# Performance work log

Measured on AMD Instinct MI355X. Metric: run time of the kernel, lower is better.

## Reference

```python
import jax, jax.numpy as jnp
import numpy as np

N, N_UP, I, L, K = 32, 16, 128, 4, 16
H_S, H_D = 4 * I, 4          # single / double stream widths (512, 4)
F_LEN = 3 * H_S + 2 * H_D    # 1544


def setup_inputs() -> dict:
    key = jax.random.key(0)
    ks = jax.random.split(key, 11)
    f32 = jnp.float32
    return {
        "electron_positions": jax.random.normal(ks[0], (N, 3), f32),
        "nuclei_positions": jax.random.normal(ks[1], (I, 3), f32),
        # torch.rand-style U[0,1) params, scaled to avoid tanh saturation / det overflow
        "v_matrices": jax.random.uniform(ks[2], (L, N, F_LEN, H_S), f32) * 1e-3,
        "b_vectors": jax.random.uniform(ks[3], (L, N, H_S), f32),
        "w_matrices": jax.random.uniform(ks[4], (L, N, N, H_D, H_D), f32) * 0.1,
        "c_vectors": jax.random.uniform(ks[5], (L, N, N, H_D), f32),
        "final_weights": jax.random.uniform(ks[6], (K, N, H_S), f32) * 1e-3,
        "final_biases": jax.random.uniform(ks[7], (K, N), f32),
        "pi_weights": jax.random.uniform(ks[8], (K, N, I), f32) * 1e-2,
        "sigma_weights": jax.random.uniform(ks[9], (K, N, I), f32),
        "omega_weights": jax.random.uniform(ks[10], (K,), f32),
    }


def _fermi_layer(V, b, W, c, sh, dh):
    # sh: [N, H_S], dh: [N, N, H_D]
    g_up = jnp.mean(sh[:N_UP], axis=0)          # [H_S]
    g_dn = jnp.mean(sh[N_UP:], axis=0)          # [H_S]
    dg_up = jnp.mean(dh[:, :N_UP], axis=1)      # [N, H_D]
    dg_dn = jnp.mean(dh[:, N_UP:], axis=1)      # [N, H_D]
    f = jnp.concatenate(
        [sh,
         jnp.broadcast_to(g_up, (N, H_S)),
         jnp.broadcast_to(g_dn, (N, H_S)),
         dg_up, dg_dn], axis=1)                 # [N, F_LEN]
    so = jnp.tanh(jnp.einsum('nfo,nf->no', V, f) + b)      # per-electron matvec
    if so.shape == sh.shape:
        so = so + sh                            # residual (shapes always match here)
    # torch bmm(W[b,i,j], h[b,j]) -> out[b,i] = sum_j W[b,i,j] h[b,j]
    do = jnp.tanh(jnp.einsum('mnij,mnj->mni', W, dh) + c)
    if do.shape == dh.shape:
        do = do + dh
    return so, do


def _forward(electron_positions, nuclei_positions, v_matrices, b_vectors,
             w_matrices, c_vectors, final_weights, final_biases,
             pi_weights, sigma_weights, omega_weights):
    eN = electron_positions[:, None, :] - nuclei_positions[None, :, :]   # [N, I, 3]
    eN_norm = jnp.linalg.norm(eN, axis=-1)                               # [N, I]
    sh = jnp.concatenate([eN.reshape(N, 3 * I), eN_norm], axis=1)        # [N, 4I]
    ee = electron_positions[:, None, :] - electron_positions[None, :, :] # [N, N, 3]
    ee_norm = jnp.linalg.norm(ee, axis=-1, keepdims=True)                # [N, N, 1]
    dh = jnp.concatenate([ee, ee_norm], axis=-1)                         # [N, N, 4]

    # Source quirk: applies layers 0..L-2, then layer L-2 again; layers[-1] unused.
    for li in list(range(L - 1)) + [L - 2]:
        sh, dh = _fermi_layer(v_matrices[li], b_vectors[li],
                              w_matrices[li], c_vectors[li], sh, dh)

    # phi[k,i,j] = (w_ki . h_j + b_ki) * sum_m pi_kim * exp(-||sigma_kim * eN_jm||)
    fd = jnp.einsum('kid,jd->kij', final_weights, sh) + final_biases[:, :, None]
    # ||sigma * v|| = |sigma| * ||v||
    env_exp = jnp.exp(-jnp.abs(sigma_weights)[:, :, None, :]
                      * eN_norm[None, None, :, :])                        # [K,N,N,I]
    env = jnp.einsum('kim,kijm->kij', pi_weights, env_exp)                # [K,N,N]
    phi = fd * env
    d_up = jnp.linalg.det(phi[:, :N_UP, :N_UP])
    d_dn = jnp.linalg.det(phi[:, N_UP:, N_UP:])
    return jnp.sum(omega_weights * d_up * d_dn)


def reference(electron_positions, nuclei_positions, v_matrices, b_vectors,
              w_matrices, c_vectors, final_weights, final_biases,
              pi_weights, sigma_weights, omega_weights):
    return _forward(electron_positions, nuclei_positions, v_matrices, b_vectors,
                    w_matrices, c_vectors, final_weights, final_biases,
                    pi_weights, sigma_weights, omega_weights)
```

## Files before the change

kernel.cpp:

```cpp
#include <hip/hip_runtime.h>
#include <math.h>

#define N_E   32
#define NUP   16
#define N_I   128
#define H_S   512
#define F_LEN 1544
#define N_K   16
#define CH    16
#define CHUNK 97

#define WS_SH    0
#define WS_DH    16384
#define WS_ENN   20480
#define WS_PART  24576
#define WS_PHI   286720
#define WS_DETS  303104

__global__ void k_init(const float* __restrict__ ep, const float* __restrict__ nuc,
                       float* __restrict__ ws) {
    float* sh  = ws + WS_SH;
    float* dh  = ws + WS_DH;
    float* eNn = ws + WS_ENN;
    int t = threadIdx.x;
    for (int idx = t; idx < N_E * N_I; idx += 256) {
        int j = idx >> 7, m = idx & 127;
        float dx = ep[j*3+0] - nuc[m*3+0];
        float dy = ep[j*3+1] - nuc[m*3+1];
        float dz = ep[j*3+2] - nuc[m*3+2];
        float nr = sqrtf(dx*dx + dy*dy + dz*dz);
        eNn[j*N_I + m] = nr;
        sh[j*H_S + 3*m + 0] = dx;
        sh[j*H_S + 3*m + 1] = dy;
        sh[j*H_S + 3*m + 2] = dz;
        sh[j*H_S + 384 + m] = nr;
    }
    for (int idx = t; idx < N_E * N_E; idx += 256) {
        int a = idx >> 5, b = idx & 31;
        float dx = ep[a*3+0] - ep[b*3+0];
        float dy = ep[a*3+1] - ep[b*3+1];
        float dz = ep[a*3+2] - ep[b*3+2];
        float nr = sqrtf(dx*dx + dy*dy + dz*dz);
        float* d = dh + (a*N_E + b)*4;
        d[0] = dx; d[1] = dy; d[2] = dz; d[3] = nr;
    }
}

__global__ __launch_bounds__(256) void k_matvec(const float* __restrict__ V,
                                                const float* __restrict__ ws,
                                                float* __restrict__ partial, int li) {
    const float* sh = ws + WS_SH;
    const float* dh = ws + WS_DH;
    __shared__ float fv[CHUNK];
    int n = blockIdx.x, ch = blockIdx.y, t = threadIdx.x;
    int f0 = ch * CHUNK;
    int flen = F_LEN - f0; if (flen > CHUNK) flen = CHUNK;

    if (t < flen) {
        int fi = f0 + t;
        float v;
        if (fi < 512) {
            v = sh[n*H_S + fi];
        } else if (fi < 1024) {
            float s = 0.f; int o = fi - 512;
            #pragma unroll
            for (int m = 0; m < 16; ++m) s += sh[m*H_S + o];
            v = s * 0.0625f;
        } else if (fi < 1536) {
            float s = 0.f; int o = fi - 1024;
            #pragma unroll
            for (int m = 16; m < 32; ++m) s += sh[m*H_S + o];
            v = s * 0.0625f;
        } else if (fi < 1540) {
            int i = fi - 1536; float s = 0.f;
            #pragma unroll
            for (int j = 0; j < 16; ++j) s += dh[(n*N_E + j)*4 + i];
            v = s * 0.0625f;
        } else {
            int i = fi - 1540; float s = 0.f;
            #pragma unroll
            for (int j = 16; j < 32; ++j) s += dh[(n*N_E + j)*4 + i];
            v = s * 0.0625f;
        }
        fv[t] = v;
    }
    __syncthreads();

    const float2* Vp = reinterpret_cast<const float2*>(
        V + ((size_t)(li*N_E + n)*F_LEN + f0)*H_S) + t;
    float ax = 0.f, ay = 0.f;
    if (flen == CHUNK) {
        #pragma unroll 8
        for (int r = 0; r < CHUNK; ++r) {
            float2 w = Vp[(size_t)r * 256];
            float fr = fv[r];
            ax = fmaf(w.x, fr, ax);
            ay = fmaf(w.y, fr, ay);
        }
    } else {
        #pragma unroll 8
        for (int r = 0; r < 89; ++r) {
            float2 w = Vp[(size_t)r * 256];
            float fr = fv[r];
            ax = fmaf(w.x, fr, ax);
            ay = fmaf(w.y, fr, ay);
        }
    }
    float2* pp = reinterpret_cast<float2*>(partial + ((size_t)n*CH + ch)*H_S) + t;
    *pp = make_float2(ax, ay);
}

__global__ __launch_bounds__(512) void k_reduce(const float* __restrict__ partial,
                                                const float* __restrict__ bv,
                                                const float* __restrict__ Wm,
                                                const float* __restrict__ cv,
                                                float* __restrict__ ws, int li) {
    float* sh = ws + WS_SH;
    float* dh = ws + WS_DH;
    int n = blockIdx.x, t = threadIdx.x;
    float s = 0.f;
    #pragma unroll
    for (int ch = 0; ch < CH; ++ch) s += partial[((size_t)n*CH + ch)*H_S + t];
    float ns = tanhf(s + bv[((size_t)li*N_E + n)*H_S + t]) + sh[n*H_S + t];

    float dval = 0.f; int j2 = 0, ii = 0;
    if (t < 128) {
        j2 = t >> 2; ii = t & 3;
        const float* Wp = Wm + ((((size_t)li*N_E + n)*N_E + j2)*4 + ii)*4;
        const float* dr = dh + (n*N_E + j2)*4;
        float acc = Wp[0]*dr[0] + Wp[1]*dr[1] + Wp[2]*dr[2] + Wp[3]*dr[3];
        dval = tanhf(acc + cv[(((size_t)li*N_E + n)*N_E + j2)*4 + ii]) + dr[ii];
    }
    __syncthreads();
    sh[n*H_S + t] = ns;
    if (t < 128) dh[(n*N_E + j2)*4 + ii] = dval;
}

__global__ __launch_bounds__(64) void k_env(const float* __restrict__ fw,
                                            const float* __restrict__ fb,
                                            const float* __restrict__ pw,
                                            const float* __restrict__ sw,
                                            const float* __restrict__ ws,
                                            float* __restrict__ phi) {
    const float* sh  = ws + WS_SH;
    const float* eNn = ws + WS_ENN;
    int ki = blockIdx.x;
    int t  = threadIdx.x;
    __shared__ float wloc[H_S];
    for (int c = t; c < H_S; c += 64) wloc[c] = fw[(size_t)ki*H_S + c];
    float p0 = pw[ki*N_I + t],            p1 = pw[ki*N_I + 64 + t];
    float s0 = fabsf(sw[ki*N_I + t]),     s1 = fabsf(sw[ki*N_I + 64 + t]);
    float fbv = fb[ki];
    __syncthreads();
    for (int j = 0; j < N_E; ++j) {
        float fd = 0.f;
        #pragma unroll
        for (int q = 0; q < 8; ++q)
            fd = fmaf(wloc[t*8 + q], sh[j*H_S + t*8 + q], fd);
        float env = p0 * expf(-s0 * eNn[j*N_I + t]) + p1 * expf(-s1 * eNn[j*N_I + 64 + t]);
        #pragma unroll
        for (int off = 32; off; off >>= 1) {
            fd  += __shfl_down(fd, off);
            env += __shfl_down(env, off);
        }
        if (t == 0) phi[(size_t)ki*N_E + j] = (fd + fbv) * env;
    }
}

__global__ __launch_bounds__(64) void k_det(const float* __restrict__ ws_phi,
                                            float* __restrict__ dets) {
    int b = blockIdx.x, k = b >> 1, sp = b & 1;
    int lane = threadIdx.x;
    int r = lane & 15;
    int base = sp ? 16 : 0;
    float a[16];
    #pragma unroll
    for (int c = 0; c < 16; ++c)
        a[c] = ws_phi[((size_t)k*N_E + base + r)*N_E + base + c];
    bool used = (lane >= 16);
    float prod = 1.f;
    int sigma[16];
    #pragma unroll
    for (int p = 0; p < 16; ++p) {
        float v = used ? -1.f : fabsf(a[p]);
        int idx = lane;
        #pragma unroll
        for (int off = 32; off; off >>= 1) {
            float ov = __shfl_xor(v, off);
            int   oi = __shfl_xor(idx, off);
            if (ov > v || (ov == v && oi < idx)) { v = ov; idx = oi; }
        }
        int q = idx;
        float pv = __shfl(a[p], q);
        prod *= pv;
        sigma[p] = q;
        float factor = (!used && lane != q && pv != 0.f) ? (a[p] / pv) : 0.f;
        #pragma unroll
        for (int c = p; c < 16; ++c) {
            float pr = __shfl(a[c], q);
            a[c] -= factor * pr;
        }
        if (lane == q) used = true;
    }
    if (lane == 0) {
        int inv = 0;
        #pragma unroll
        for (int x = 0; x < 16; ++x)
            #pragma unroll
            for (int y = x + 1; y < 16; ++y) inv += (sigma[x] > sigma[y]) ? 1 : 0;
        dets[b] = prod * ((inv & 1) ? -1.f : 1.f);
    }
}

__global__ void k_out(const float* __restrict__ dets, const float* __restrict__ omega,
                      float* __restrict__ out) {
    if (threadIdx.x == 0) {
        float s = 0.f;
        for (int k = 0; k < N_K; ++k)
            s += omega[k] * dets[2*k + 0] * dets[2*k + 1];
        out[0] = s;
    }
}

extern "C" void kernel_launch(void* const* d_in, const int* in_sizes, int n_in,
                              void* d_out, int out_size, void* d_ws, size_t ws_size,
                              hipStream_t stream) {
    const float* ep  = (const float*)d_in[0];
    const float* nuc = (const float*)d_in[1];
    const float* V   = (const float*)d_in[2];
    const float* bv  = (const float*)d_in[3];
    const float* Wm  = (const float*)d_in[4];
    const float* cv  = (const float*)d_in[5];
    const float* fw  = (const float*)d_in[6];
    const float* fb  = (const float*)d_in[7];
    const float* pw  = (const float*)d_in[8];
    const float* sw  = (const float*)d_in[9];
    const float* om  = (const float*)d_in[10];
    float* out = (float*)d_out;
    float* ws  = (float*)d_ws;

    float* partial = ws + WS_PART;
    float* phi     = ws + WS_PHI;
    float* dets    = ws + WS_DETS;

    k_init<<<dim3(1), dim3(256), 0, stream>>>(ep, nuc, ws);

    for (int a = 0; a < 4; ++a) {
        int li = (a < 3) ? a : 2;
        k_matvec<<<dim3(N_E, CH), dim3(256), 0, stream>>>(V, ws, partial, li);
        k_reduce<<<dim3(N_E), dim3(512), 0, stream>>>(partial, bv, Wm, cv, ws, li);
    }

    k_env<<<dim3(N_K * N_E), dim3(64), 0, stream>>>(fw, fb, pw, sw, ws, phi);
    k_det<<<dim3(2 * N_K), dim3(64), 0, stream>>>(phi, dets);
    k_out<<<dim3(1), dim3(64), 0, stream>>>(dets, om, out);
}
```

Before: 139.3 us.

## Split matvec across row-waves and column halves; fuse envelope with determinant

The per-electron matvec now splits each chunk's columns into two halves on a third grid dimension. Within a block, four waves stride over rows and each thread loads a float4. This doubles the block count and raises per-thread load width to improve bandwidth use on the large V stream. Each chunk now writes four wave partials instead of one, so the reduce kernel sums 64 partials per output instead of 16. The envelope and orbital-product kernel is fused with the determinant kernel: each of the 32 blocks computes only the 16x16 diagonal block it needs into shared memory, skipping the off-diagonal phi entries and one launch plus a global round trip.

```diff
diff --git a/kernel.cpp b/kernel.cpp
--- a/kernel.cpp
+++ b/kernel.cpp
@@ -14,8 +14,7 @@
 #define WS_DH    16384
 #define WS_ENN   20480
 #define WS_PART  24576
-#define WS_PHI   286720
-#define WS_DETS  303104
+#define WS_DETS  (24576 + 64*32*512)
 
 __global__ void k_init(const float* __restrict__ ep, const float* __restrict__ nuc,
                        float* __restrict__ ws) {
@@ -52,7 +51,7 @@
     const float* sh = ws + WS_SH;
     const float* dh = ws + WS_DH;
     __shared__ float fv[CHUNK];
-    int n = blockIdx.x, ch = blockIdx.y, t = threadIdx.x;
+    int n = blockIdx.x, ch = blockIdx.y, half = blockIdx.z, t = threadIdx.x;
     int f0 = ch * CHUNK;
     int flen = F_LEN - f0; if (flen > CHUNK) flen = CHUNK;
 
@@ -86,28 +85,23 @@
     }
     __syncthreads();
 
-    const float2* Vp = reinterpret_cast<const float2*>(
-        V + ((size_t)(li*N_E + n)*F_LEN + f0)*H_S) + t;
-    float ax = 0.f, ay = 0.f;
-    if (flen == CHUNK) {
-        #pragma unroll 8
-        for (int r = 0; r < CHUNK; ++r) {
-            float2 w = Vp[(size_t)r * 256];
-            float fr = fv[r];
-            ax = fmaf(w.x, fr, ax);
-            ay = fmaf(w.y, fr, ay);
-        }
-    } else {
-        #pragma unroll 8
-        for (int r = 0; r < 89; ++r) {
-            float2 w = Vp[(size_t)r * 256];
-            float fr = fv[r];
-            ax = fmaf(w.x, fr, ax);
-            ay = fmaf(w.y, fr, ay);
-        }
-    }
-    float2* pp = reinterpret_cast<float2*>(partial + ((size_t)n*CH + ch)*H_S) + t;
-    *pp = make_float2(ax, ay);
+    int w  = t >> 6;
+    int c4 = t & 63;
+    const float* Vbase = V + ((size_t)(li*N_E + n)*F_LEN + f0)*H_S
+                           + half*256 + c4*4;
+    float a0 = 0.f, a1 = 0.f, a2 = 0.f, a3 = 0.f;
+    #pragma unroll 8
+    for (int r = w; r < flen; r += 4) {
+        float4 wv = *reinterpret_cast<const float4*>(Vbase + (size_t)r * H_S);
+        float fr = fv[r];
+        a0 = fmaf(wv.x, fr, a0);
+        a1 = fmaf(wv.y, fr, a1);
+        a2 = fmaf(wv.z, fr, a2);
+        a3 = fmaf(wv.w, fr, a3);
+    }
+    float4* pp = reinterpret_cast<float4*>(
+        partial + (((size_t)(ch*4 + w))*N_E + n)*H_S + half*256) + c4;
+    *pp = make_float4(a0, a1, a2, a3);
 }
 
 __global__ __launch_bounds__(512) void k_reduce(const float* __restrict__ partial,
@@ -119,8 +113,9 @@
     float* dh = ws + WS_DH;
     int n = blockIdx.x, t = threadIdx.x;
     float s = 0.f;
-    #pragma unroll
-    for (int ch = 0; ch < CH; ++ch) s += partial[((size_t)n*CH + ch)*H_S + t];
+    #pragma unroll 16
+    for (int sl = 0; sl < 64; ++sl)
+        s += partial[((size_t)sl*N_E + n)*H_S + t];
     float ns = tanhf(s + bv[((size_t)li*N_E + n)*H_S + t]) + sh[n*H_S + t];
 
     float dval = 0.f; int j2 = 0, ii = 0;
@@ -136,79 +131,81 @@
     if (t < 128) dh[(n*N_E + j2)*4 + ii] = dval;
 }
 
-__global__ __launch_bounds__(64) void k_env(const float* __restrict__ fw,
-                                            const float* __restrict__ fb,
-                                            const float* __restrict__ pw,
-                                            const float* __restrict__ sw,
-                                            const float* __restrict__ ws,
-                                            float* __restrict__ phi) {
+__global__ __launch_bounds__(256) void k_envdet(const float* __restrict__ fw,
+                                                const float* __restrict__ fb,
+                                                const float* __restrict__ pw,
+                                                const float* __restrict__ sw,
+                                                const float* __restrict__ ws,
+                                                float* __restrict__ dets) {
     const float* sh  = ws + WS_SH;
     const float* eNn = ws + WS_ENN;
-    int ki = blockIdx.x;
-    int t  = threadIdx.x;
-    __shared__ float wloc[H_S];
-    for (int c = t; c < H_S; c += 64) wloc[c] = fw[(size_t)ki*H_S + c];
-    float p0 = pw[ki*N_I + t],            p1 = pw[ki*N_I + 64 + t];
-    float s0 = fabsf(sw[ki*N_I + t]),     s1 = fabsf(sw[ki*N_I + 64 + t]);
-    float fbv = fb[ki];
+    int b = blockIdx.x, k = b >> 1, sp = b & 1, base = sp * 16;
+    int t = threadIdx.x;
+    int i = base + (t >> 4);
+    int j = base + (t & 15);
+
+    const float* wv = fw + ((size_t)k*N_E + i)*H_S;
+    const float* sv = sh + (size_t)j*H_S;
+    float fd = 0.f;
+    #pragma unroll 8
+    for (int c = 0; c < H_S; c += 4) {
+        float4 a  = *reinterpret_cast<const float4*>(wv + c);
+        float4 bz = *reinterpret_cast<const float4*>(sv + c);
+        fd += a.x*bz.x + a.y*bz.y + a.z*bz.z + a.w*bz.w;
+    }
+    fd += fb[k*N_E + i];
+
+    const float* pv = pw + ((size_t)k*N_E + i)*N_I;
+    const float* sg = sw + ((size_t)k*N_E + i)*N_I;
+    const float* rn = eNn + (size_t)j*N_I;
+    float env = 0.f;
+    #pragma unroll 4
+    for (int m = 0; m < N_I; ++m)
+        env = fmaf(pv[m], expf(-fabsf(sg[m]) * rn[m]), env);
+
+    __shared__ float phi[16][16];
+    phi[t >> 4][t & 15] = fd * env;
     __syncthreads();
-    for (int j = 0; j < N_E; ++j) {
-        float fd = 0.f;
+
+    if (t < 64) {
+        int lane = t;
+        int r = lane & 15;
+        float a[16];
         #pragma unroll
-        for (int q = 0; q < 8; ++q)
-            fd = fmaf(wloc[t*8 + q], sh[j*H_S + t*8 + q], fd);
-        float env = p0 * expf(-s0 * eNn[j*N_I + t]) + p1 * expf(-s1 * eNn[j*N_I + 64 + t]);
+        for (int c = 0; c < 16; ++c) a[c] = phi[r][c];
+        bool used = (lane >= 16);
+        float prod = 1.f;
+        int sigma[16];
         #pragma unroll
-        for (int off = 32; off; off >>= 1) {
-            fd  += __shfl_down(fd, off);
-            env += __shfl_down(env, off);
+        for (int p = 0; p < 16; ++p) {
+            float v = used ? -1.f : fabsf(a[p]);
+            int idx = lane;
+            #pragma unroll
+            for (int off = 32; off; off >>= 1) {
+                float ov = __shfl_xor(v, off);
+                int   oi = __shfl_xor(idx, off);
+                if (ov > v || (ov == v && oi < idx)) { v = ov; idx = oi; }
+            }
+            int q = idx;
+            float pvt = __shfl(a[p], q);
+            prod *= pvt;
+            sigma[p] = q;
+            float factor = (!used && lane != q && pvt != 0.f) ? (a[p] / pvt) : 0.f;
+            #pragma unroll
+            for (int c = p; c < 16; ++c) {
+                float pr = __shfl(a[c], q);
+                a[c] -= factor * pr;
+            }
+            if (lane == q) used = true;
         }
-        if (t == 0) phi[(size_t)ki*N_E + j] = (fd + fbv) * env;
-    }
-}
-
-__global__ __launch_bounds__(64) void k_det(const float* __restrict__ ws_phi,
-                                            float* __restrict__ dets) {
-    int b = blockIdx.x, k = b >> 1, sp = b & 1;
-    int lane = threadIdx.x;
-    int r = lane & 15;
-    int base = sp ? 16 : 0;
-    float a[16];
-    #pragma unroll
-    for (int c = 0; c < 16; ++c)
-        a[c] = ws_phi[((size_t)k*N_E + base + r)*N_E + base + c];
-    bool used = (lane >= 16);
-    float prod = 1.f;
-    int sigma[16];
-    #pragma unroll
-    for (int p = 0; p < 16; ++p) {
-        float v = used ? -1.f : fabsf(a[p]);
-        int idx = lane;
-        #pragma unroll
-        for (int off = 32; off; off >>= 1) {
-            float ov = __shfl_xor(v, off);
-            int   oi = __shfl_xor(idx, off);
-            if (ov > v || (ov == v && oi < idx)) { v = ov; idx = oi; }
+        if (lane == 0) {
+            int inv = 0;
+            #pragma unroll
+            for (int x = 0; x < 16; ++x)
+                #pragma unroll
+                for (int y = x + 1; y < 16; ++y) inv += (sigma[x] > sigma[y]) ? 1 : 0;
+            dets[b] = prod * ((inv & 1) ? -1.f : 1.f);
         }
-        int q = idx;
-        float pv = __shfl(a[p], q);
-        prod *= pv;
-        sigma[p] = q;
-        float factor = (!used && lane != q && pv != 0.f) ? (a[p] / pv) : 0.f;
-        #pragma unroll
-        for (int c = p; c < 16; ++c) {
-            float pr = __shfl(a[c], q);
-            a[c] -= factor * pr;
-        }
-        if (lane == q) used = true;
-    }
-    if (lane == 0) {
-        int inv = 0;
-        #pragma unroll
-        for (int x = 0; x < 16; ++x)
-            #pragma unroll
-            for (int y = x + 1; y < 16; ++y) inv += (sigma[x] > sigma[y]) ? 1 : 0;
-        dets[b] = prod * ((inv & 1) ? -1.f : 1.f);
     }
 }
 
@@ -240,18 +237,16 @@
     float* ws  = (float*)d_ws;
 
     float* partial = ws + WS_PART;
-    float* phi     = ws + WS_PHI;
     float* dets    = ws + WS_DETS;
 
     k_init<<<dim3(1), dim3(256), 0, stream>>>(ep, nuc, ws);
 
     for (int a = 0; a < 4; ++a) {
         int li = (a < 3) ? a : 2;
-        k_matvec<<<dim3(N_E, CH), dim3(256), 0, stream>>>(V, ws, partial, li);
+        k_matvec<<<dim3(N_E, CH, 2), dim3(256), 0, stream>>>(V, ws, partial, li);
         k_reduce<<<dim3(N_E), dim3(512), 0, stream>>>(partial, bv, Wm, cv, ws, li);
     }
 
-    k_env<<<dim3(N_K * N_E), dim3(64), 0, stream>>>(fw, fb, pw, sw, ws, phi);
-    k_det<<<dim3(2 * N_K), dim3(64), 0, stream>>>(phi, dets);
+    k_envdet<<<dim3(2 * N_K), dim3(256), 0, stream>>>(fw, fb, pw, sw, ws, dets);
     k_out<<<dim3(1), dim3(64), 0, stream>>>(dets, om, out);
 }
```

Result: slower. 145.3 us (+4.3%).
